# Optimization experiments

Measured on AMD Instinct MI355X. Metric: run time of the kernel, lower is better.

## Reference

```python
import jax, jax.numpy as jnp
import numpy as np

H = 96  # hidden_dim


def _rbf(dist):
    # GaussianSmearing(start=0, stop=10, num_gaussians=16)
    offset = jnp.linspace(0.0, 10.0, 16, dtype=dist.dtype)
    coeff = -0.5 / (10.0 / 15.0) ** 2
    d = dist[:, None] - offset[None, :]
    return jnp.exp(coeff * d * d)


def _gatv2(s, edge, edge_attr, Wl, bl, Wr, br, We, att, bias):
    # PyG GATv2Conv, heads=1: e = leaky_relu(lin_l(x_src)+lin_r(x_tgt)+lin_edge(ea));
    # alpha = segment_softmax(e @ att, tgt); out = scatter_sum(alpha * lin_l(x_src)) + bias
    N = s.shape[0]
    src, tgt = edge[0], edge[1]
    xl = s @ Wl + bl
    xr = s @ Wr + br
    e = jax.nn.leaky_relu(xl[src] + xr[tgt] + edge_attr @ We, 0.2)  # [E,H]
    logits = e @ att  # [E]
    m = jax.ops.segment_max(logits, tgt, num_segments=N)
    a = jnp.exp(logits - m[tgt])
    denom = jax.ops.segment_sum(a, tgt, num_segments=N)
    alpha = a / denom[tgt]
    out = jax.ops.segment_sum(alpha[:, None] * xl[src], tgt, num_segments=N)
    return out + bias


def _encoder(x, edge, pos, Wemb, bemb, gp):
    s0 = x @ Wemb + bemb                      # [N,H]
    s = jax.nn.silu(s0)
    row, col = edge[0], edge[1]
    dist = jnp.linalg.norm(pos[row] - pos[col], axis=-1)
    ea = _rbf(dist)                           # [E,16]
    s = s + jax.nn.silu(_gatv2(s, edge, ea, *gp))
    v = s0.reshape(x.shape[0], -1, 3)[:, :16, :]  # [N,16,3]
    return s, v


def _forward(x_L, pos_L, x_P, pos_P, edge_L, edge_P, cross_src, cross_tgt,
             Wemb_L, bemb_L, Wl_L, bl_L, Wr_L, br_L, We_L, att_L, bias_L,
             Wemb_P, bemb_P, Wl_P, bl_P, Wr_P, br_P, We_P, att_P, bias_P,
             Win, b_in, Wout, bout, Wq, bq, Wk, bk, Wv, bv, W1, b1, W2, b2):
    s_L, v_L = _encoder(x_L, edge_L, pos_L, Wemb_L, bemb_L,
                        (Wl_L, bl_L, Wr_L, br_L, We_L, att_L, bias_L))
    s_P, v_P = _encoder(x_P, edge_P, pos_P, Wemb_P, bemb_P,
                        (Wl_P, bl_P, Wr_P, br_P, We_P, att_P, bias_P))
    # CausalMolSSM: x + out_proj(silu(in_proj(x)).chunk(2)[0])
    h = jax.nn.silu(s_L @ Win + b_in)[:, : 2 * H]
    s_L = s_L + h @ Wout + bout
    # GVPCrossAttention: per-edge gather, global softmax (dim=0 in source), scatter-add
    q = (s_L @ Wq + bq)[cross_tgt]
    k = (s_P @ Wk + bk)[cross_src]
    logits = jnp.sum(q * k, axis=-1) / 8.0     # [E_X]
    attn = jax.nn.softmax(logits, axis=0)      # global softmax over all edges (as in source)
    vmsg = (s_P @ Wv + bv)[cross_src]
    s_L = s_L.at[cross_tgt].add(attn[:, None] * vmsg)
    # head
    return jax.nn.silu(s_L @ W1 + b1) @ W2 + b2  # v_pred [N_L,3]


def setup_inputs() -> dict:
    N_L, N_P = 8192, 32768
    E_L, E_P, E_X = 262144, 524288, 262144
    D_L, D_P = 167, 21
    ks = iter(jax.random.split(jax.random.key(0), 64))

    def w(shape, fan):
        return (jax.random.normal(next(ks), shape, dtype=jnp.float32) / np.sqrt(fan)).astype(jnp.float32)

    inp = {}
    inp['x_L'] = jax.random.normal(next(ks), (N_L, D_L), dtype=jnp.float32)
    inp['pos_L'] = jax.random.normal(next(ks), (N_L, 3), dtype=jnp.float32)
    inp['x_P'] = jax.random.normal(next(ks), (N_P, D_P), dtype=jnp.float32)
    inp['pos_P'] = jax.random.normal(next(ks), (N_P, 3), dtype=jnp.float32)
    inp['edge_L'] = jax.random.randint(next(ks), (2, E_L), 0, N_L)
    inp['edge_P'] = jax.random.randint(next(ks), (2, E_P), 0, N_P)
    inp['cross_src'] = jax.random.randint(next(ks), (E_X,), 0, N_P)
    inp['cross_tgt'] = jax.random.randint(next(ks), (E_X,), 0, N_L)
    for pre, din in (('L', D_L), ('P', D_P)):
        inp[f'Wemb_{pre}'] = w((din, H), din); inp[f'bemb_{pre}'] = w((H,), din)
        inp[f'Wl_{pre}'] = w((H, H), H); inp[f'bl_{pre}'] = w((H,), H)
        inp[f'Wr_{pre}'] = w((H, H), H); inp[f'br_{pre}'] = w((H,), H)
        inp[f'We_{pre}'] = w((16, H), 16)
        inp[f'att_{pre}'] = w((H,), H)
        inp[f'bias_{pre}'] = w((H,), H)
    inp['Win'] = w((H, 4 * H), H); inp['b_in'] = w((4 * H,), H)
    inp['Wout'] = w((2 * H, H), 2 * H); inp['bout'] = w((H,), 2 * H)
    for n in ('q', 'k', 'v'):
        inp[f'W{n}'] = w((H, H), H); inp[f'b{n}'] = w((H,), H)
    inp['W1'] = w((H, H), H); inp['b1'] = w((H,), H)
    inp['W2'] = w((H, 3), H); inp['b2'] = w((3,), H)
    return inp


def reference(x_L, pos_L, x_P, pos_P, edge_L, edge_P, cross_src, cross_tgt,
              Wemb_L, bemb_L, Wl_L, bl_L, Wr_L, br_L, We_L, att_L, bias_L,
              Wemb_P, bemb_P, Wl_P, bl_P, Wr_P, br_P, We_P, att_P, bias_P,
              Win, b_in, Wout, bout, Wq, bq, Wk, bk, Wv, bv, W1, b1, W2, b2):
    return _forward(x_L, pos_L, x_P, pos_P, edge_L, edge_P, cross_src, cross_tgt,
                    Wemb_L, bemb_L, Wl_L, bl_L, Wr_L, br_L, We_L, att_L, bias_L,
                    Wemb_P, bemb_P, Wl_P, bl_P, Wr_P, br_P, We_P, att_P, bias_P,
                    Win, b_in, Wout, bout, Wq, bq, Wk, bk, Wv, bv, W1, b1, W2, b2)
```

## Files before the change

kernel.cpp:

```cpp
#include <hip/hip_runtime.h>

__device__ __forceinline__ float silu_f(float x) { return x / (1.f + __expf(-x)); }

__device__ __forceinline__ void atomicMaxF(float* addr, float val) {
    if (val >= 0.f) atomicMax((int*)addr, __float_as_int(val));
    else            atomicMin((unsigned int*)addr, __float_as_uint(val));
}

__device__ __forceinline__ unsigned short f2bf(float x) {
    unsigned int u = __float_as_uint(x);
    return (unsigned short)((u + 0x7fffu + ((u >> 16) & 1u)) >> 16);
}
__device__ __forceinline__ float bf2f(unsigned short h) {
    return __uint_as_float(((unsigned int)h) << 16);
}
__device__ __forceinline__ float bf_lo(unsigned int u) { return __uint_as_float(u << 16); }
__device__ __forceinline__ float bf_hi(unsigned int u) { return __uint_as_float(u & 0xffff0000u); }
__device__ __forceinline__ float bfdot(unsigned int a, unsigned int b) {
    return bf_lo(a) * bf_lo(b) + bf_hi(a) * bf_hi(b);
}

__global__ void fill_i(int* __restrict__ p, int v, int n) {
    int i = blockIdx.x * blockDim.x + threadIdx.x;
    if (i < n) p[i] = v;
}

__global__ __launch_bounds__(256) void hist_all_kernel(const int* __restrict__ tgtL,
        const int* __restrict__ tgtP, const int* __restrict__ ctgt, int* __restrict__ count,
        int E_L, int E_P, int E_X, int N_L, int N_P) {
    int e = blockIdx.x * blockDim.x + threadIdx.x;
    if (e < E_L) atomicAdd(&count[tgtL[e]], 1);
    else if (e < E_L + E_P) atomicAdd(&count[N_L + tgtP[e - E_L]], 1);
    else if (e < E_L + E_P + E_X) atomicAdd(&count[N_L + N_P + ctgt[e - E_L - E_P]], 1);
}

__global__ __launch_bounds__(256) void scan_blocksum_kernel(const int* __restrict__ count,
                                                            int* __restrict__ bsum, int n) {
    int b = blockIdx.x, t = threadIdx.x;
    int base = b * 4096 + t * 16;
    int s = 0;
#pragma unroll
    for (int k = 0; k < 16; ++k) {
        int idx = base + k;
        s += (idx < n) ? count[idx] : 0;
    }
#pragma unroll
    for (int off = 1; off < 64; off <<= 1) s += __shfl_xor(s, off, 64);
    __shared__ int ws[4];
    int lane = t & 63, wid = t >> 6;
    if (lane == 0) ws[wid] = s;
    __syncthreads();
    if (t == 0) bsum[b] = ws[0] + ws[1] + ws[2] + ws[3];
}

__global__ void scan_top_kernel(int* __restrict__ bsum, int nb, float* __restrict__ csc) {
    if (threadIdx.x == 0) {
        int run = 0;
        for (int i = 0; i < nb; ++i) { int c = bsum[i]; bsum[i] = run; run += c; }
        csc[0] = -3.4e38f; csc[1] = 0.f;
    }
}

__global__ __launch_bounds__(256) void scan_apply_kernel(const int* __restrict__ count,
        const int* __restrict__ bsum, int* __restrict__ rowptr, int* __restrict__ cursor,
        int n, int E) {
    int b = blockIdx.x, t = threadIdx.x;
    int base = b * 4096 + t * 16;
    int v[16];
    int s = 0;
#pragma unroll
    for (int k = 0; k < 16; ++k) {
        int idx = base + k;
        v[k] = (idx < n) ? count[idx] : 0;
        s += v[k];
    }
    int lane = t & 63, wid = t >> 6;
    int inc = s;
#pragma unroll
    for (int off = 1; off < 64; off <<= 1) {
        int o = __shfl_up(inc, off, 64);
        if (lane >= off) inc += o;
    }
    __shared__ int ws[4];
    if (lane == 63) ws[wid] = inc;
    __syncthreads();
    int woff = 0;
    for (int w = 0; w < wid; ++w) woff += ws[w];
    int prefix = bsum[b] + woff + (inc - s);
#pragma unroll
    for (int k = 0; k < 16; ++k) {
        int idx = base + k;
        if (idx < n) { rowptr[idx] = prefix; cursor[idx] = prefix; prefix += v[k]; }
    }
    if (b == 0 && t == 0) rowptr[n] = E;
}

__global__ __launch_bounds__(256) void pre_all_kernel(const int* __restrict__ eL,
        const int* __restrict__ eP, const int* __restrict__ csrc, const int* __restrict__ ctgt,
        const float* __restrict__ posL, const float* __restrict__ posP,
        int* __restrict__ cursor, unsigned int* __restrict__ sdp,
        int E_L, int E_P, int E_X, int N_L, int N_P) {
    int e = blockIdx.x * blockDim.x + threadIdx.x;
    if (e >= E_L + E_P + E_X) return;
    unsigned int pack;
    int node;
    if (e < E_L + E_P) {
        const int* ed; const float* pos; int idx, E, nbase;
        if (e < E_L) { ed = eL; pos = posL; idx = e; E = E_L; nbase = 0; }
        else         { ed = eP; pos = posP; idx = e - E_L; E = E_P; nbase = N_L; }
        int si = ed[idx], ti = ed[E + idx];
        node = nbase + ti;
        float dx = pos[si * 3 + 0] - pos[ti * 3 + 0];
        float dy = pos[si * 3 + 1] - pos[ti * 3 + 1];
        float dz = pos[si * 3 + 2] - pos[ti * 3 + 2];
        float dist = sqrtf(dx * dx + dy * dy + dz * dz);
        int dq = min((int)(dist * 4096.f), 65535);
        pack = (unsigned int)(si + nbase) | ((unsigned int)dq << 16);
    } else {
        int idx = e - E_L - E_P;
        int ti = ctgt[idx];
        pack = (unsigned int)csrc[idx] | ((unsigned int)ti << 16);
        node = N_L + N_P + ti;
    }
    int p = atomicAdd(&cursor[node], 1);
    sdp[p] = pack;
}

__global__ __launch_bounds__(96) void rbf_table_pack_kernel(const float* __restrict__ We_L,
        const float* __restrict__ We_P, unsigned int* __restrict__ T2_L,
        unsigned int* __restrict__ T2_P) {
    int b = blockIdx.x;
    const float* We = (b < 1024) ? We_L : We_P;
    unsigned int* T2 = (b < 1024) ? T2_L : T2_P;
    int i = (b < 1024) ? b : b - 1024;
    int h = threadIdx.x;
    float d0 = (float)i * 0.015625f, d1 = (float)(i + 1) * 0.015625f;
    float a0 = 0.f, a1 = 0.f;
#pragma unroll
    for (int g = 0; g < 16; ++g) {
        float w = We[g * 96 + h];
        float t0 = d0 - 0.66666667f * (float)g;
        float t1 = d1 - 0.66666667f * (float)g;
        a0 += __expf(-1.125f * t0 * t0) * w;
        a1 += __expf(-1.125f * t1 * t1) * w;
    }
    T2[i * 96 + h] = (unsigned int)f2bf(a0) | ((unsigned int)f2bf(a1 - a0) << 16);
}

__global__ __launch_bounds__(256) void gat_all_kernel(const int* __restrict__ rowptr,
        const unsigned int* __restrict__ sdp, const unsigned short* __restrict__ xlb,
        const float* __restrict__ xr,
        const unsigned int* __restrict__ T2_L, const unsigned int* __restrict__ T2_P,
        const float* __restrict__ att_L, const float* __restrict__ att_P,
        const float* __restrict__ bias_L, const float* __restrict__ bias_P,
        float* __restrict__ s_L, float* __restrict__ s_P, int N_L, int Ncomb) {
    int tid = threadIdx.x;
    int l = tid & 31;
    int n = blockIdx.x * 8 + (tid >> 5);
    if (n >= Ncomb) return;
    bool isL = n < N_L;
    const unsigned int* T2 = isL ? T2_L : T2_P;
    const float* att = isL ? att_L : att_P;
    const float* bias = isL ? bias_L : bias_P;
    float* srow = isL ? (s_L + (size_t)n * 96) : (s_P + (size_t)(n - N_L) * 96);
    float att0 = att[l], att1 = att[32 + l], att2 = att[64 + l];
    size_t nb = (size_t)n * 96;
    float xr0 = xr[nb + l], xr1 = xr[nb + 32 + l], xr2 = xr[nb + 64 + l];
    int beg = rowptr[n], end = rowptr[n + 1];
    float m = -3.4e38f, d = 0.f, a0 = 0.f, a1 = 0.f, a2 = 0.f;
    for (int j = beg; j < end; j += 4) {
        unsigned int tp0[4], tp1[4], tp2[4];
        unsigned short xs0[4], xs1[4], xs2[4];
        float ff[4];
#pragma unroll
        for (int k = 0; k < 4; ++k) {
            int jj = min(j + k, end - 1);
            unsigned int u = sdp[jj];
            int src = (int)(u & 0xffffu);
            int dq = (int)(u >> 16);
            int i = dq >> 6;
            ff[k] = (float)(dq & 63) * 0.015625f;
            const unsigned int* tr = T2 + (size_t)i * 96;
            tp0[k] = tr[l]; tp1[k] = tr[32 + l]; tp2[k] = tr[64 + l];
            const unsigned short* xp = xlb + (size_t)src * 96;
            xs0[k] = xp[l]; xs1[k] = xp[32 + l]; xs2[k] = xp[64 + l];
        }
        float y0[4], y1[4], y2[4], lt[4];
#pragma unroll
        for (int k = 0; k < 4; ++k) {
            y0[k] = bf2f(xs0[k]); y1[k] = bf2f(xs1[k]); y2[k] = bf2f(xs2[k]);
            float v0 = y0[k] + xr0 + bf_lo(tp0[k]) + ff[k] * bf_hi(tp0[k]);
            float v1 = y1[k] + xr1 + bf_lo(tp1[k]) + ff[k] * bf_hi(tp1[k]);
            float v2 = y2[k] + xr2 + bf_lo(tp2[k]) + ff[k] * bf_hi(tp2[k]);
            v0 = fmaxf(v0, 0.f) + 0.2f * fminf(v0, 0.f);
            v1 = fmaxf(v1, 0.f) + 0.2f * fminf(v1, 0.f);
            v2 = fmaxf(v2, 0.f) + 0.2f * fminf(v2, 0.f);
            float t = v0 * att0 + v1 * att1 + v2 * att2;
#pragma unroll
            for (int off = 1; off < 32; off <<= 1) t += __shfl_xor(t, off, 64);
            lt[k] = (j + k < end) ? t : -3.4e38f;
        }
        float bm = fmaxf(fmaxf(lt[0], lt[1]), fmaxf(lt[2], lt[3]));
        float nm = fmaxf(m, bm);
        float sc = __expf(m - nm);
        d *= sc; a0 *= sc; a1 *= sc; a2 *= sc;
#pragma unroll
        for (int k = 0; k < 4; ++k) {
            float w = __expf(lt[k] - nm);
            d += w;
            a0 += w * y0[k]; a1 += w * y1[k]; a2 += w * y2[k];
        }
        m = nm;
    }
    float agg0 = (d > 0.f) ? a0 / d : 0.f;
    float agg1 = (d > 0.f) ? a1 / d : 0.f;
    float agg2 = (d > 0.f) ? a2 / d : 0.f;
    srow[l]      += silu_f(agg0 + bias[l]);
    srow[32 + l] += silu_f(agg1 + bias[32 + l]);
    srow[64 + l] += silu_f(agg2 + bias[64 + l]);
}

__global__ __launch_bounds__(256) void cross_logit_e_kernel(const unsigned int* __restrict__ sdX,
        const unsigned short* __restrict__ qnb, const unsigned short* __restrict__ knb,
        float* __restrict__ clog_s, float* __restrict__ csc, int E) {
    int e = blockIdx.x * blockDim.x + threadIdx.x;
    float logit = -3.4e38f;
    if (e < E) {
        unsigned int u = sdX[e];
        int src = (int)(u & 0xffffu);
        int tgt = (int)(u >> 16);
        const uint4* q4 = (const uint4*)(qnb + (size_t)tgt * 96);
        const uint4* k4 = (const uint4*)(knb + (size_t)src * 96);
        float acc = 0.f;
#pragma unroll
        for (int i = 0; i < 12; ++i) {
            uint4 qa = q4[i], ka = k4[i];
            acc += bfdot(qa.x, ka.x) + bfdot(qa.y, ka.y) + bfdot(qa.z, ka.z) + bfdot(qa.w, ka.w);
        }
        logit = acc * 0.125f;
        clog_s[e] = logit;
    }
    __shared__ float red[256];
    red[threadIdx.x] = logit; __syncthreads();
    for (int s = 128; s > 0; s >>= 1) {
        if (threadIdx.x < s) red[threadIdx.x] = fmaxf(red[threadIdx.x], red[threadIdx.x + s]);
        __syncthreads();
    }
    if (threadIdx.x == 0) atomicMaxF(&csc[0], red[0]);
}

__global__ __launch_bounds__(256) void cross_denom_kernel(const float* __restrict__ clog_s,
                                                          float* __restrict__ csc, int E) {
    int e = blockIdx.x * blockDim.x + threadIdx.x;
    float a = 0.f;
    float mg = csc[0];
    if (e < E) a = __expf(clog_s[e] - mg);
    __shared__ float red[256];
    red[threadIdx.x] = a; __syncthreads();
    for (int s = 128; s > 0; s >>= 1) {
        if (threadIdx.x < s) red[threadIdx.x] += red[threadIdx.x + s];
        __syncthreads();
    }
    if (threadIdx.x == 0) atomicAdd(&csc[1], red[0]);
}

__global__ __launch_bounds__(256) void cross_apply_v4_kernel(const int* __restrict__ rowptr,
        const unsigned int* __restrict__ sdp, const float* __restrict__ clog_s,
        const unsigned short* __restrict__ vnb, const float* __restrict__ csc,
        float* __restrict__ sL, int N, int baseX) {
    int tid = threadIdx.x;
    int l = tid & 31;
    int n = blockIdx.x * 8 + (tid >> 5);
    if (n >= N) return;
    int beg = rowptr[n], end = rowptr[n + 1];
    if (beg == end) return;
    float M = csc[0], invD = 1.f / csc[1];
    float a0 = 0.f, a1 = 0.f, a2 = 0.f;
    for (int j = beg; j < end; j += 4) {
        unsigned short v0[4], v1[4], v2[4]; float w[4];
#pragma unroll
        for (int k = 0; k < 4; ++k) {
            int jj = min(j + k, end - 1);
            int src = (int)(sdp[jj] & 0xffffu);
            const unsigned short* vp = vnb + (size_t)src * 96;
            v0[k] = vp[l]; v1[k] = vp[32 + l]; v2[k] = vp[64 + l];
            w[k] = (j + k < end) ? __expf(clog_s[jj - baseX] - M) : 0.f;
        }
#pragma unroll
        for (int k = 0; k < 4; ++k) {
            a0 += w[k] * bf2f(v0[k]); a1 += w[k] * bf2f(v1[k]); a2 += w[k] * bf2f(v2[k]);
        }
    }
    size_t nb = (size_t)n * 96;
    sL[nb + l]      += a0 * invD;
    sL[nb + 32 + l] += a1 * invD;
    sL[nb + 64 + l] += a2 * invD;
}


__global__ __launch_bounds__(192) void enc_all_kernel(
        const float* __restrict__ x_L, const float* __restrict__ x_P,
        const float* __restrict__ WembL, const float* __restrict__ bembL,
        const float* __restrict__ WembP, const float* __restrict__ bembP,
        const float* __restrict__ WlL, const float* __restrict__ blL,
        const float* __restrict__ WrL, const float* __restrict__ brL,
        const float* __restrict__ WlP, const float* __restrict__ blP,
        const float* __restrict__ WrP, const float* __restrict__ brP,
        float* __restrict__ s_L, float* __restrict__ s_P,
        unsigned short* __restrict__ xlb, float* __restrict__ xr,
        int N_L, int N_P, int D_L, int D_P, int BL) {
    __shared__ float xs[16 * 167];
    __shared__ float ss[16 * 96];
    int b = blockIdx.x;
    bool isL = b < BL;
    const float* x    = isL ? x_L : x_P;
    const float* Wemb = isL ? WembL : WembP;
    const float* bemb = isL ? bembL : bembP;
    const float* Wl   = isL ? WlL : WlP;
    const float* bl   = isL ? blL : blP;
    const float* Wr   = isL ? WrL : WrP;
    const float* br   = isL ? brL : brP;
    float* sOut = isL ? s_L : s_P;
    int N = isL ? N_L : N_P;
    int D = isL ? D_L : D_P;
    int n0 = (isL ? b : b - BL) * 16;
    int cbase = isL ? 0 : N_L;
    int t = threadIdx.x, half = t / 96, h = t - half * 96;
    for (int i = t; i < 16 * D; i += 192) {
        int r = i / D, dd = i - r * D, nn = n0 + r;
        xs[i] = (nn < N) ? x[(size_t)nn * D + dd] : 0.f;
    }
    __syncthreads();
    float acc[8]; float bb = bemb[h];
#pragma unroll
    for (int r = 0; r < 8; ++r) acc[r] = bb;
    const float* xp = &xs[half * 8 * D];
    for (int dd = 0; dd < D; ++dd) {
        float w = Wemb[dd * 96 + h];
#pragma unroll
        for (int r = 0; r < 8; ++r) acc[r] += xp[r * D + dd] * w;
    }
#pragma unroll
    for (int r = 0; r < 8; ++r) {
        int nn = n0 + half * 8 + r;
        float v = silu_f(acc[r]);
        if (nn < N) sOut[(size_t)nn * 96 + h] = v;
        ss[(half * 8 + r) * 96 + h] = v;
    }
    __syncthreads();
    const float* sp = &ss[half * 8 * 96];
    float a1[8], a2[8];
    float bb1 = bl[h], bb2 = br[h];
#pragma unroll
    for (int r = 0; r < 8; ++r) { a1[r] = bb1; a2[r] = bb2; }
    for (int k = 0; k < 96; ++k) {
        float w1 = Wl[k * 96 + h], w2 = Wr[k * 96 + h];
#pragma unroll
        for (int r = 0; r < 8; ++r) { float v = sp[r * 96 + k]; a1[r] += v * w1; a2[r] += v * w2; }
    }
#pragma unroll
    for (int r = 0; r < 8; ++r) {
        int nn = n0 + half * 8 + r;
        if (nn < N) {
            xlb[(size_t)(cbase + nn) * 96 + h] = f2bf(a1[r]);
            xr[(size_t)(cbase + nn) * 96 + h] = a2[r];
        }
    }
}

__global__ __launch_bounds__(192) void qkv_all_kernel(
        const float* __restrict__ s_L, const float* __restrict__ s_P,
        const float* __restrict__ Wq, const float* __restrict__ bq,
        const float* __restrict__ Wk, const float* __restrict__ bk,
        const float* __restrict__ Wv, const float* __restrict__ bv,
        unsigned short* __restrict__ qnb, unsigned short* __restrict__ knb,
        unsigned short* __restrict__ vnb, int N_L, int N_P, int BL) {
    __shared__ float xs[16 * 96];
    int b = blockIdx.x;
    bool isL = b < BL;
    const float* s = isL ? s_L : s_P;
    int N = isL ? N_L : N_P;
    int n0 = (isL ? b : b - BL) * 16;
    int t = threadIdx.x, half = t / 96, h = t - half * 96;
    for (int i = t; i < 16 * 96; i += 192) {
        int r = i / 96, c = i - r * 96, nn = n0 + r;
        xs[i] = (nn < N) ? s[(size_t)nn * 96 + c] : 0.f;
    }
    __syncthreads();
    const float* xp = &xs[half * 8 * 96];
    if (isL) {
        float a1[8]; float bb1 = bq[h];
#pragma unroll
        for (int r = 0; r < 8; ++r) a1[r] = bb1;
        for (int k = 0; k < 96; ++k) {
            float w1 = Wq[k * 96 + h];
#pragma unroll
            for (int r = 0; r < 8; ++r) a1[r] += xp[r * 96 + k] * w1;
        }
#pragma unroll
        for (int r = 0; r < 8; ++r) {
            int nn = n0 + half * 8 + r;
            if (nn < N) qnb[(size_t)nn * 96 + h] = f2bf(a1[r]);
        }
    } else {
        float a1[8], a2[8];
        float bb1 = bk[h], bb2 = bv[h];
#pragma unroll
        for (int r = 0; r < 8; ++r) { a1[r] = bb1; a2[r] = bb2; }
        for (int k = 0; k < 96; ++k) {
            float w1 = Wk[k * 96 + h], w2 = Wv[k * 96 + h];
#pragma unroll
            for (int r = 0; r < 8; ++r) { float v = xp[r * 96 + k]; a1[r] += v * w1; a2[r] += v * w2; }
        }
#pragma unroll
        for (int r = 0; r < 8; ++r) {
            int nn = n0 + half * 8 + r;
            if (nn < N) {
                knb[(size_t)nn * 96 + h] = f2bf(a1[r]);
                vnb[(size_t)nn * 96 + h] = f2bf(a2[r]);
            }
        }
    }
}

__global__ __launch_bounds__(192) void ssm2_kernel(float* __restrict__ sL,
        const float* __restrict__ Win, const float* __restrict__ b_in,
        const float* __restrict__ Wout, const float* __restrict__ bout, int N) {
    __shared__ float row[4 * 96];
    __shared__ float u[4 * 192];
    __shared__ float pu[4 * 96];
    int t = threadIdx.x;
    int n0 = blockIdx.x * 4;
    for (int i = t; i < 4 * 96; i += 192) {
        int r = i / 96, c = i - r * 96, nn = n0 + r;
        row[i] = (nn < N) ? sL[(size_t)nn * 96 + c] : 0.f;
    }
    __syncthreads();
    float acc[4]; float bb = b_in[t];
#pragma unroll
    for (int r = 0; r < 4; ++r) acc[r] = bb;
    for (int k = 0; k < 96; ++k) {
        float w = Win[k * 384 + t];
#pragma unroll
        for (int r = 0; r < 4; ++r) acc[r] += row[r * 96 + k] * w;
    }
#pragma unroll
    for (int r = 0; r < 4; ++r) u[r * 192 + t] = silu_f(acc[r]);
    __syncthreads();
    int half = t / 96, h = t - half * 96;
    float d[4] = {0.f, 0.f, 0.f, 0.f};
    int j0 = half * 96;
    for (int j = j0; j < j0 + 96; ++j) {
        float w = Wout[j * 96 + h];
#pragma unroll
        for (int r = 0; r < 4; ++r) d[r] += u[r * 192 + j] * w;
    }
    if (half == 1) {
#pragma unroll
        for (int r = 0; r < 4; ++r) pu[r * 96 + h] = d[r];
    }
    __syncthreads();
    if (half == 0) {
        float bo = bout[h];
#pragma unroll
        for (int r = 0; r < 4; ++r) {
            int nn = n0 + r;
            if (nn < N) sL[(size_t)nn * 96 + h] = row[r * 96 + h] + bo + d[r] + pu[r * 96 + h];
        }
    }
}

__global__ __launch_bounds__(192) void head2_kernel(const float* __restrict__ sL,
        const float* __restrict__ W1, const float* __restrict__ b1,
        const float* __restrict__ W2, const float* __restrict__ b2,
        float* __restrict__ out, int N) {
    __shared__ float buf[16 * 96];
    int t = threadIdx.x, half = t / 96, h = t - half * 96;
    int n0 = blockIdx.x * 16;
    for (int i = t; i < 16 * 96; i += 192) {
        int r = i / 96, c = i - r * 96, nn = n0 + r;
        buf[i] = (nn < N) ? sL[(size_t)nn * 96 + c] : 0.f;
    }
    __syncthreads();
    int rbase = half * 8;
    float a[8]; float bb = b1[h];
#pragma unroll
    for (int r = 0; r < 8; ++r) a[r] = bb;
    for (int k = 0; k < 96; ++k) {
        float w = W1[k * 96 + h];
#pragma unroll
        for (int r = 0; r < 8; ++r) a[r] += buf[(rbase + r) * 96 + k] * w;
    }
    __syncthreads();
#pragma unroll
    for (int r = 0; r < 8; ++r) buf[(rbase + r) * 96 + h] = silu_f(a[r]);
    __syncthreads();
    if (t < 48) {
        int r = t / 3, c = t - r * 3;
        float o = b2[c];
        for (int j = 0; j < 96; ++j) o += buf[r * 96 + j] * W2[j * 3 + c];
        int nn = n0 + r;
        if (nn < N) out[nn * 3 + c] = o;
    }
}

static inline int cdiv(int a, int b) { return (a + b - 1) / b; }

extern "C" void kernel_launch(void* const* d_in, const int* in_sizes, int n_in,
                              void* d_out, int out_size, void* d_ws, size_t ws_size,
                              hipStream_t stream) {
    const float* x_L   = (const float*)d_in[0];
    const float* pos_L = (const float*)d_in[1];
    const float* x_P   = (const float*)d_in[2];
    const float* pos_P = (const float*)d_in[3];
    const int* edge_L = (const int*)d_in[4];
    const int* edge_P = (const int*)d_in[5];
    const int* csrc   = (const int*)d_in[6];
    const int* ctgt   = (const int*)d_in[7];
    const float *Wemb_L = (const float*)d_in[8],  *bemb_L = (const float*)d_in[9];
    const float *Wl_L = (const float*)d_in[10], *bl_L = (const float*)d_in[11];
    const float *Wr_L = (const float*)d_in[12], *br_L = (const float*)d_in[13];
    const float *We_L = (const float*)d_in[14], *att_L = (const float*)d_in[15], *bias_L = (const float*)d_in[16];
    const float *Wemb_P = (const float*)d_in[17], *bemb_P = (const float*)d_in[18];
    const float *Wl_P = (const float*)d_in[19], *bl_P = (const float*)d_in[20];
    const float *Wr_P = (const float*)d_in[21], *br_P = (const float*)d_in[22];
    const float *We_P = (const float*)d_in[23], *att_P = (const float*)d_in[24], *bias_P = (const float*)d_in[25];
    const float *Win = (const float*)d_in[26], *b_in = (const float*)d_in[27];
    const float *Wout = (const float*)d_in[28], *bout = (const float*)d_in[29];
    const float *Wq = (const float*)d_in[30], *bq = (const float*)d_in[31];
    const float *Wk = (const float*)d_in[32], *bk = (const float*)d_in[33];
    const float *Wv = (const float*)d_in[34], *bv = (const float*)d_in[35];
    const float *W1 = (const float*)d_in[36], *b1 = (const float*)d_in[37];
    const float *W2 = (const float*)d_in[38], *b2 = (const float*)d_in[39];

    const int N_L = in_sizes[1] / 3;
    const int N_P = in_sizes[3] / 3;
    const int E_L = in_sizes[4] / 2;
    const int E_P = in_sizes[5] / 2;
    const int E_X = in_sizes[6];
    const int D_L = in_sizes[0] / N_L;
    const int D_P = in_sizes[2] / N_P;
    const int Ncomb = N_L + N_P;
    const int Ntot = N_L + N_P + N_L;
    const int Etot = E_L + E_P + E_X;
    const int baseX = E_L + E_P;

    float* ws = (float*)d_ws;
    float*          s_L    = ws;
    float*          s_P    = s_L + (size_t)N_L * 96;
    float*          xr     = s_P + (size_t)N_P * 96;
    unsigned short* xlb    = (unsigned short*)(xr + (size_t)Ncomb * 96);
    unsigned short* knb    = xlb + (size_t)Ncomb * 96;
    unsigned short* vnb    = knb + (size_t)N_P * 96;
    unsigned short* qnb    = vnb + (size_t)N_P * 96;
    unsigned int*   sdp    = (unsigned int*)(qnb + (size_t)N_L * 96);
    float*          clog_s = (float*)(sdp + (size_t)Etot);
    unsigned int*   T2_L   = (unsigned int*)(clog_s + (size_t)E_X);
    unsigned int*   T2_P   = T2_L + 1024 * 96;
    int*            rowptr = (int*)(T2_P + 1024 * 96);
    int*            count  = rowptr + (size_t)Ntot + 1;
    int*            cursor = count + (size_t)Ntot;
    float*          csc    = (float*)(cursor + (size_t)Ntot);
    int*            bsum   = (int*)(csc + 2);

    const int BL = cdiv(N_L, 16), BP = cdiv(N_P, 16);

    rbf_table_pack_kernel<<<2048, 96, 0, stream>>>(We_L, We_P, T2_L, T2_P);
    fill_i<<<cdiv(Ntot, 256), 256, 0, stream>>>(count, 0, Ntot);
    hist_all_kernel<<<cdiv(Etot, 256), 256, 0, stream>>>(edge_L + E_L, edge_P + E_P, ctgt,
        count, E_L, E_P, E_X, N_L, N_P);
    scan_blocksum_kernel<<<cdiv(Ntot, 4096), 256, 0, stream>>>(count, bsum, Ntot);
    scan_top_kernel<<<1, 64, 0, stream>>>(bsum, cdiv(Ntot, 4096), csc);
    scan_apply_kernel<<<cdiv(Ntot, 4096), 256, 0, stream>>>(count, bsum, rowptr, cursor, Ntot, Etot);
    pre_all_kernel<<<cdiv(Etot, 256), 256, 0, stream>>>(edge_L, edge_P, csrc, ctgt,
        pos_L, pos_P, cursor, sdp, E_L, E_P, E_X, N_L, N_P);

    enc_all_kernel<<<BL + BP, 192, 0, stream>>>(x_L, x_P, Wemb_L, bemb_L, Wemb_P, bemb_P,
        Wl_L, bl_L, Wr_L, br_L, Wl_P, bl_P, Wr_P, br_P,
        s_L, s_P, xlb, xr, N_L, N_P, D_L, D_P, BL);

    gat_all_kernel<<<cdiv(Ncomb, 8), 256, 0, stream>>>(rowptr, sdp, xlb, xr, T2_L, T2_P,
        att_L, att_P, bias_L, bias_P, s_L, s_P, N_L, Ncomb);

    ssm2_kernel<<<cdiv(N_L, 4), 192, 0, stream>>>(s_L, Win, b_in, Wout, bout, N_L);

    qkv_all_kernel<<<BL + BP, 192, 0, stream>>>(s_L, s_P, Wq, bq, Wk, bk, Wv, bv,
        qnb, knb, vnb, N_L, N_P, BL);
    cross_logit_e_kernel<<<cdiv(E_X, 256), 256, 0, stream>>>(sdp + (size_t)baseX, qnb, knb,
        clog_s, csc, E_X);
    cross_denom_kernel<<<cdiv(E_X, 256), 256, 0, stream>>>(clog_s, csc, E_X);
    cross_apply_v4_kernel<<<cdiv(N_L, 8), 256, 0, stream>>>(rowptr + N_L + N_P, sdp,
        clog_s, vnb, csc, s_L, N_L, baseX);

    head2_kernel<<<cdiv(N_L, 16), 192, 0, stream>>>(s_L, W1, b1, W2, b2, (float*)d_out, N_L);
}
```

Baseline: 505.4 us.

## Register-tile dense node GEMMs 4x4 with float4 weights; store xr as bf16

Rewrites the per-node dense matmul kernels (encoder, qkv, SSM, head) so each thread computes a 4-row by 4-column register tile using float4 weight loads, with 32 nodes per block instead of 16. The SSM kernel now handles 8 rows per block and no longer splits the output projection across two halves with a shared-memory reduction. The xr projection is stored as bf16 instead of fp32, which halves its memory traffic in the GAT kernel at some cost in precision. Larger tiles cut redundant weight loads but leave fewer blocks, which may reduce occupancy at small node counts.

Measured after the change: 466.5 us. -7.7%, faster.

```diff
diff --git a/kernel.cpp b/kernel.cpp
--- a/kernel.cpp
+++ b/kernel.cpp
@@ -149,7 +149,7 @@
 
 __global__ __launch_bounds__(256) void gat_all_kernel(const int* __restrict__ rowptr,
         const unsigned int* __restrict__ sdp, const unsigned short* __restrict__ xlb,
-        const float* __restrict__ xr,
+        const unsigned short* __restrict__ xrb,
         const unsigned int* __restrict__ T2_L, const unsigned int* __restrict__ T2_P,
         const float* __restrict__ att_L, const float* __restrict__ att_P,
         const float* __restrict__ bias_L, const float* __restrict__ bias_P,
@@ -165,7 +165,7 @@
     float* srow = isL ? (s_L + (size_t)n * 96) : (s_P + (size_t)(n - N_L) * 96);
     float att0 = att[l], att1 = att[32 + l], att2 = att[64 + l];
     size_t nb = (size_t)n * 96;
-    float xr0 = xr[nb + l], xr1 = xr[nb + 32 + l], xr2 = xr[nb + 64 + l];
+    float xr0 = bf2f(xrb[nb + l]), xr1 = bf2f(xrb[nb + 32 + l]), xr2 = bf2f(xrb[nb + 64 + l]);
     int beg = rowptr[n], end = rowptr[n + 1];
     float m = -3.4e38f, d = 0.f, a0 = 0.f, a1 = 0.f, a2 = 0.f;
     for (int j = beg; j < end; j += 4) {
@@ -307,10 +307,10 @@
         const float* __restrict__ WlP, const float* __restrict__ blP,
         const float* __restrict__ WrP, const float* __restrict__ brP,
         float* __restrict__ s_L, float* __restrict__ s_P,
-        unsigned short* __restrict__ xlb, float* __restrict__ xr,
+        unsigned short* __restrict__ xlb, unsigned short* __restrict__ xrb,
         int N_L, int N_P, int D_L, int D_P, int BL) {
-    __shared__ float xs[16 * 167];
-    __shared__ float ss[16 * 96];
+    __shared__ float xs[32 * 167];
+    __shared__ float ss[32 * 96];
     int b = blockIdx.x;
     bool isL = b < BL;
     const float* x    = isL ? x_L : x_P;
@@ -323,47 +323,65 @@
     float* sOut = isL ? s_L : s_P;
     int N = isL ? N_L : N_P;
     int D = isL ? D_L : D_P;
-    int n0 = (isL ? b : b - BL) * 16;
+    int n0 = (isL ? b : b - BL) * 32;
     int cbase = isL ? 0 : N_L;
-    int t = threadIdx.x, half = t / 96, h = t - half * 96;
-    for (int i = t; i < 16 * D; i += 192) {
+    int t = threadIdx.x;
+    int hg = t % 24, h4 = hg * 4;
+    int rg = t / 24;
+    for (int i = t; i < 32 * D; i += 192) {
         int r = i / D, dd = i - r * D, nn = n0 + r;
         xs[i] = (nn < N) ? x[(size_t)nn * D + dd] : 0.f;
     }
     __syncthreads();
-    float acc[8]; float bb = bemb[h];
-#pragma unroll
-    for (int r = 0; r < 8; ++r) acc[r] = bb;
-    const float* xp = &xs[half * 8 * D];
+    float4 be = *(const float4*)&bemb[h4];
+    float acc[4][4];
+#pragma unroll
+    for (int r = 0; r < 4; ++r) { acc[r][0] = be.x; acc[r][1] = be.y; acc[r][2] = be.z; acc[r][3] = be.w; }
+    const float* xrow = &xs[rg * 4 * D];
     for (int dd = 0; dd < D; ++dd) {
-        float w = Wemb[dd * 96 + h];
-#pragma unroll
-        for (int r = 0; r < 8; ++r) acc[r] += xp[r * D + dd] * w;
-    }
-#pragma unroll
-    for (int r = 0; r < 8; ++r) {
-        int nn = n0 + half * 8 + r;
-        float v = silu_f(acc[r]);
-        if (nn < N) sOut[(size_t)nn * 96 + h] = v;
-        ss[(half * 8 + r) * 96 + h] = v;
-    }
-    __syncthreads();
-    const float* sp = &ss[half * 8 * 96];
-    float a1[8], a2[8];
-    float bb1 = bl[h], bb2 = br[h];
-#pragma unroll
-    for (int r = 0; r < 8; ++r) { a1[r] = bb1; a2[r] = bb2; }
+        float4 w = *(const float4*)&Wemb[dd * 96 + h4];
+#pragma unroll
+        for (int r = 0; r < 4; ++r) {
+            float xv = xrow[r * D + dd];
+            acc[r][0] += xv * w.x; acc[r][1] += xv * w.y;
+            acc[r][2] += xv * w.z; acc[r][3] += xv * w.w;
+        }
+    }
+#pragma unroll
+    for (int r = 0; r < 4; ++r) {
+        int row = rg * 4 + r, nn = n0 + row;
+        float4 v = make_float4(silu_f(acc[r][0]), silu_f(acc[r][1]),
+                               silu_f(acc[r][2]), silu_f(acc[r][3]));
+        *(float4*)&ss[row * 96 + h4] = v;
+        if (nn < N) *(float4*)&sOut[(size_t)nn * 96 + h4] = v;
+    }
+    __syncthreads();
+    float4 b1v = *(const float4*)&bl[h4];
+    float4 b2v = *(const float4*)&br[h4];
+    float a1[4][4], a2[4][4];
+#pragma unroll
+    for (int r = 0; r < 4; ++r) {
+        a1[r][0] = b1v.x; a1[r][1] = b1v.y; a1[r][2] = b1v.z; a1[r][3] = b1v.w;
+        a2[r][0] = b2v.x; a2[r][1] = b2v.y; a2[r][2] = b2v.z; a2[r][3] = b2v.w;
+    }
+    const float* srow = &ss[rg * 4 * 96];
     for (int k = 0; k < 96; ++k) {
-        float w1 = Wl[k * 96 + h], w2 = Wr[k * 96 + h];
-#pragma unroll
-        for (int r = 0; r < 8; ++r) { float v = sp[r * 96 + k]; a1[r] += v * w1; a2[r] += v * w2; }
-    }
-#pragma unroll
-    for (int r = 0; r < 8; ++r) {
-        int nn = n0 + half * 8 + r;
+        float4 w1 = *(const float4*)&Wl[k * 96 + h4];
+        float4 w2 = *(const float4*)&Wr[k * 96 + h4];
+#pragma unroll
+        for (int r = 0; r < 4; ++r) {
+            float xv = srow[r * 96 + k];
+            a1[r][0] += xv * w1.x; a1[r][1] += xv * w1.y; a1[r][2] += xv * w1.z; a1[r][3] += xv * w1.w;
+            a2[r][0] += xv * w2.x; a2[r][1] += xv * w2.y; a2[r][2] += xv * w2.z; a2[r][3] += xv * w2.w;
+        }
+    }
+#pragma unroll
+    for (int r = 0; r < 4; ++r) {
+        int nn = n0 + rg * 4 + r;
         if (nn < N) {
-            xlb[(size_t)(cbase + nn) * 96 + h] = f2bf(a1[r]);
-            xr[(size_t)(cbase + nn) * 96 + h] = a2[r];
+            size_t o = (size_t)(cbase + nn) * 96 + h4;
+            *(ushort4*)&xlb[o] = make_ushort4(f2bf(a1[r][0]), f2bf(a1[r][1]), f2bf(a1[r][2]), f2bf(a1[r][3]));
+            *(ushort4*)&xrb[o] = make_ushort4(f2bf(a2[r][0]), f2bf(a2[r][1]), f2bf(a2[r][2]), f2bf(a2[r][3]));
         }
     }
 }
@@ -375,130 +393,171 @@
         const float* __restrict__ Wv, const float* __restrict__ bv,
         unsigned short* __restrict__ qnb, unsigned short* __restrict__ knb,
         unsigned short* __restrict__ vnb, int N_L, int N_P, int BL) {
-    __shared__ float xs[16 * 96];
+    __shared__ float xs[32 * 96];
     int b = blockIdx.x;
     bool isL = b < BL;
     const float* s = isL ? s_L : s_P;
     int N = isL ? N_L : N_P;
-    int n0 = (isL ? b : b - BL) * 16;
-    int t = threadIdx.x, half = t / 96, h = t - half * 96;
-    for (int i = t; i < 16 * 96; i += 192) {
+    int n0 = (isL ? b : b - BL) * 32;
+    int t = threadIdx.x;
+    int hg = t % 24, h4 = hg * 4;
+    int rg = t / 24;
+    for (int i = t; i < 32 * 96; i += 192) {
         int r = i / 96, c = i - r * 96, nn = n0 + r;
         xs[i] = (nn < N) ? s[(size_t)nn * 96 + c] : 0.f;
     }
     __syncthreads();
-    const float* xp = &xs[half * 8 * 96];
+    const float* srow = &xs[rg * 4 * 96];
     if (isL) {
-        float a1[8]; float bb1 = bq[h];
-#pragma unroll
-        for (int r = 0; r < 8; ++r) a1[r] = bb1;
+        float4 bb = *(const float4*)&bq[h4];
+        float a1[4][4];
+#pragma unroll
+        for (int r = 0; r < 4; ++r) { a1[r][0] = bb.x; a1[r][1] = bb.y; a1[r][2] = bb.z; a1[r][3] = bb.w; }
         for (int k = 0; k < 96; ++k) {
-            float w1 = Wq[k * 96 + h];
-#pragma unroll
-            for (int r = 0; r < 8; ++r) a1[r] += xp[r * 96 + k] * w1;
-        }
-#pragma unroll
-        for (int r = 0; r < 8; ++r) {
-            int nn = n0 + half * 8 + r;
-            if (nn < N) qnb[(size_t)nn * 96 + h] = f2bf(a1[r]);
+            float4 w = *(const float4*)&Wq[k * 96 + h4];
+#pragma unroll
+            for (int r = 0; r < 4; ++r) {
+                float xv = srow[r * 96 + k];
+                a1[r][0] += xv * w.x; a1[r][1] += xv * w.y; a1[r][2] += xv * w.z; a1[r][3] += xv * w.w;
+            }
+        }
+#pragma unroll
+        for (int r = 0; r < 4; ++r) {
+            int nn = n0 + rg * 4 + r;
+            if (nn < N)
+                *(ushort4*)&qnb[(size_t)nn * 96 + h4] =
+                    make_ushort4(f2bf(a1[r][0]), f2bf(a1[r][1]), f2bf(a1[r][2]), f2bf(a1[r][3]));
         }
     } else {
-        float a1[8], a2[8];
-        float bb1 = bk[h], bb2 = bv[h];
-#pragma unroll
-        for (int r = 0; r < 8; ++r) { a1[r] = bb1; a2[r] = bb2; }
+        float4 bb1 = *(const float4*)&bk[h4];
+        float4 bb2 = *(const float4*)&bv[h4];
+        float a1[4][4], a2[4][4];
+#pragma unroll
+        for (int r = 0; r < 4; ++r) {
+            a1[r][0] = bb1.x; a1[r][1] = bb1.y; a1[r][2] = bb1.z; a1[r][3] = bb1.w;
+            a2[r][0] = bb2.x; a2[r][1] = bb2.y; a2[r][2] = bb2.z; a2[r][3] = bb2.w;
+        }
         for (int k = 0; k < 96; ++k) {
-            float w1 = Wk[k * 96 + h], w2 = Wv[k * 96 + h];
-#pragma unroll
-            for (int r = 0; r < 8; ++r) { float v = xp[r * 96 + k]; a1[r] += v * w1; a2[r] += v * w2; }
-        }
-#pragma unroll
-        for (int r = 0; r < 8; ++r) {
-            int nn = n0 + half * 8 + r;
+            float4 w1 = *(const float4*)&Wk[k * 96 + h4];
+            float4 w2 = *(const float4*)&Wv[k * 96 + h4];
+#pragma unroll
+            for (int r = 0; r < 4; ++r) {
+                float xv = srow[r * 96 + k];
+                a1[r][0] += xv * w1.x; a1[r][1] += xv * w1.y; a1[r][2] += xv * w1.z; a1[r][3] += xv * w1.w;
+                a2[r][0] += xv * w2.x; a2[r][1] += xv * w2.y; a2[r][2] += xv * w2.z; a2[r][3] += xv * w2.w;
+            }
+        }
+#pragma unroll
+        for (int r = 0; r < 4; ++r) {
+            int nn = n0 + rg * 4 + r;
             if (nn < N) {
-                knb[(size_t)nn * 96 + h] = f2bf(a1[r]);
-                vnb[(size_t)nn * 96 + h] = f2bf(a2[r]);
+                *(ushort4*)&knb[(size_t)nn * 96 + h4] =
+                    make_ushort4(f2bf(a1[r][0]), f2bf(a1[r][1]), f2bf(a1[r][2]), f2bf(a1[r][3]));
+                *(ushort4*)&vnb[(size_t)nn * 96 + h4] =
+                    make_ushort4(f2bf(a2[r][0]), f2bf(a2[r][1]), f2bf(a2[r][2]), f2bf(a2[r][3]));
             }
         }
     }
 }
 
-__global__ __launch_bounds__(192) void ssm2_kernel(float* __restrict__ sL,
+__global__ __launch_bounds__(192) void ssm3_kernel(float* __restrict__ sL,
         const float* __restrict__ Win, const float* __restrict__ b_in,
         const float* __restrict__ Wout, const float* __restrict__ bout, int N) {
-    __shared__ float row[4 * 96];
-    __shared__ float u[4 * 192];
-    __shared__ float pu[4 * 96];
+    __shared__ float row[8 * 96];
+    __shared__ float u[8 * 192];
     int t = threadIdx.x;
-    int n0 = blockIdx.x * 4;
-    for (int i = t; i < 4 * 96; i += 192) {
+    int n0 = blockIdx.x * 8;
+    for (int i = t; i < 8 * 96; i += 192) {
         int r = i / 96, c = i - r * 96, nn = n0 + r;
         row[i] = (nn < N) ? sL[(size_t)nn * 96 + c] : 0.f;
     }
     __syncthreads();
-    float acc[4]; float bb = b_in[t];
-#pragma unroll
-    for (int r = 0; r < 4; ++r) acc[r] = bb;
-    for (int k = 0; k < 96; ++k) {
-        float w = Win[k * 384 + t];
-#pragma unroll
-        for (int r = 0; r < 4; ++r) acc[r] += row[r * 96 + k] * w;
-    }
-#pragma unroll
-    for (int r = 0; r < 4; ++r) u[r * 192 + t] = silu_f(acc[r]);
-    __syncthreads();
-    int half = t / 96, h = t - half * 96;
-    float d[4] = {0.f, 0.f, 0.f, 0.f};
-    int j0 = half * 96;
-    for (int j = j0; j < j0 + 96; ++j) {
-        float w = Wout[j * 96 + h];
-#pragma unroll
-        for (int r = 0; r < 4; ++r) d[r] += u[r * 192 + j] * w;
-    }
-    if (half == 1) {
-#pragma unroll
-        for (int r = 0; r < 4; ++r) pu[r * 96 + h] = d[r];
-    }
-    __syncthreads();
-    if (half == 0) {
-        float bo = bout[h];
-#pragma unroll
-        for (int r = 0; r < 4; ++r) {
-            int nn = n0 + r;
-            if (nn < N) sL[(size_t)nn * 96 + h] = row[r * 96 + h] + bo + d[r] + pu[r * 96 + h];
-        }
-    }
-}
-
-__global__ __launch_bounds__(192) void head2_kernel(const float* __restrict__ sL,
+    {
+        int cg = t % 48, c4 = cg * 4;
+        int rg = t / 48;
+        float4 bb = *(const float4*)&b_in[c4];
+        float a[2][4];
+#pragma unroll
+        for (int r = 0; r < 2; ++r) { a[r][0] = bb.x; a[r][1] = bb.y; a[r][2] = bb.z; a[r][3] = bb.w; }
+        const float* rr = &row[rg * 2 * 96];
+        for (int k = 0; k < 96; ++k) {
+            float4 w = *(const float4*)&Win[k * 384 + c4];
+#pragma unroll
+            for (int r = 0; r < 2; ++r) {
+                float xv = rr[r * 96 + k];
+                a[r][0] += xv * w.x; a[r][1] += xv * w.y; a[r][2] += xv * w.z; a[r][3] += xv * w.w;
+            }
+        }
+#pragma unroll
+        for (int r = 0; r < 2; ++r) {
+            int ro = rg * 2 + r;
+            u[ro * 192 + c4 + 0] = silu_f(a[r][0]);
+            u[ro * 192 + c4 + 1] = silu_f(a[r][1]);
+            u[ro * 192 + c4 + 2] = silu_f(a[r][2]);
+            u[ro * 192 + c4 + 3] = silu_f(a[r][3]);
+        }
+    }
+    __syncthreads();
+    {
+        int hg = t % 24, h4 = hg * 4;
+        int rg2 = t / 24;
+        float4 bb = *(const float4*)&bout[h4];
+        float a[4] = {bb.x, bb.y, bb.z, bb.w};
+        const float* ur = &u[rg2 * 192];
+        for (int j = 0; j < 192; ++j) {
+            float4 w = *(const float4*)&Wout[j * 96 + h4];
+            float uv = ur[j];
+            a[0] += uv * w.x; a[1] += uv * w.y; a[2] += uv * w.z; a[3] += uv * w.w;
+        }
+        int nn = n0 + rg2;
+        if (nn < N) {
+            float4 rv = *(const float4*)&row[rg2 * 96 + h4];
+            *(float4*)&sL[(size_t)nn * 96 + h4] =
+                make_float4(rv.x + a[0], rv.y + a[1], rv.z + a[2], rv.w + a[3]);
+        }
+    }
+}
+
+__global__ __launch_bounds__(192) void head3_kernel(const float* __restrict__ sL,
         const float* __restrict__ W1, const float* __restrict__ b1,
         const float* __restrict__ W2, const float* __restrict__ b2,
         float* __restrict__ out, int N) {
-    __shared__ float buf[16 * 96];
-    int t = threadIdx.x, half = t / 96, h = t - half * 96;
-    int n0 = blockIdx.x * 16;
-    for (int i = t; i < 16 * 96; i += 192) {
+    __shared__ float buf[32 * 96];
+    __shared__ float tt[32 * 96];
+    int t = threadIdx.x;
+    int n0 = blockIdx.x * 32;
+    for (int i = t; i < 32 * 96; i += 192) {
         int r = i / 96, c = i - r * 96, nn = n0 + r;
         buf[i] = (nn < N) ? sL[(size_t)nn * 96 + c] : 0.f;
     }
     __syncthreads();
-    int rbase = half * 8;
-    float a[8]; float bb = b1[h];
-#pragma unroll
-    for (int r = 0; r < 8; ++r) a[r] = bb;
+    int hg = t % 24, h4 = hg * 4;
+    int rg = t / 24;
+    float4 bb = *(const float4*)&b1[h4];
+    float a[4][4];
+#pragma unroll
+    for (int r = 0; r < 4; ++r) { a[r][0] = bb.x; a[r][1] = bb.y; a[r][2] = bb.z; a[r][3] = bb.w; }
+    const float* srow = &buf[rg * 4 * 96];
     for (int k = 0; k < 96; ++k) {
-        float w = W1[k * 96 + h];
-#pragma unroll
-        for (int r = 0; r < 8; ++r) a[r] += buf[(rbase + r) * 96 + k] * w;
-    }
-    __syncthreads();
-#pragma unroll
-    for (int r = 0; r < 8; ++r) buf[(rbase + r) * 96 + h] = silu_f(a[r]);
-    __syncthreads();
-    if (t < 48) {
+        float4 w = *(const float4*)&W1[k * 96 + h4];
+#pragma unroll
+        for (int r = 0; r < 4; ++r) {
+            float xv = srow[r * 96 + k];
+            a[r][0] += xv * w.x; a[r][1] += xv * w.y; a[r][2] += xv * w.z; a[r][3] += xv * w.w;
+        }
+    }
+#pragma unroll
+    for (int r = 0; r < 4; ++r) {
+        int row = rg * 4 + r;
+        *(float4*)&tt[row * 96 + h4] = make_float4(silu_f(a[r][0]), silu_f(a[r][1]),
+                                                   silu_f(a[r][2]), silu_f(a[r][3]));
+    }
+    __syncthreads();
+    if (t < 96) {
         int r = t / 3, c = t - r * 3;
         float o = b2[c];
-        for (int j = 0; j < 96; ++j) o += buf[r * 96 + j] * W2[j * 3 + c];
+        const float* tr = &tt[r * 96];
+        for (int j = 0; j < 96; ++j) o += tr[j] * W2[j * 3 + c];
         int nn = n0 + r;
         if (nn < N) out[nn * 3 + c] = o;
     }
@@ -548,8 +607,8 @@
     float* ws = (float*)d_ws;
     float*          s_L    = ws;
     float*          s_P    = s_L + (size_t)N_L * 96;
-    float*          xr     = s_P + (size_t)N_P * 96;
-    unsigned short* xlb    = (unsigned short*)(xr + (size_t)Ncomb * 96);
+    unsigned short* xrb    = (unsigned short*)(s_P + (size_t)N_P * 96);
+    unsigned short* xlb    = xrb + (size_t)Ncomb * 96;
     unsigned short* knb    = xlb + (size_t)Ncomb * 96;
     unsigned short* vnb    = knb + (size_t)N_P * 96;
     unsigned short* qnb    = vnb + (size_t)N_P * 96;
@@ -563,7 +622,7 @@
     float*          csc    = (float*)(cursor + (size_t)Ntot);
     int*            bsum   = (int*)(csc + 2);
 
-    const int BL = cdiv(N_L, 16), BP = cdiv(N_P, 16);
+    const int BL = cdiv(N_L, 32), BP = cdiv(N_P, 32);
 
     rbf_table_pack_kernel<<<2048, 96, 0, stream>>>(We_L, We_P, T2_L, T2_P);
     fill_i<<<cdiv(Ntot, 256), 256, 0, stream>>>(count, 0, Ntot);
@@ -577,12 +636,12 @@
 
     enc_all_kernel<<<BL + BP, 192, 0, stream>>>(x_L, x_P, Wemb_L, bemb_L, Wemb_P, bemb_P,
         Wl_L, bl_L, Wr_L, br_L, Wl_P, bl_P, Wr_P, br_P,
-        s_L, s_P, xlb, xr, N_L, N_P, D_L, D_P, BL);
-
-    gat_all_kernel<<<cdiv(Ncomb, 8), 256, 0, stream>>>(rowptr, sdp, xlb, xr, T2_L, T2_P,
+        s_L, s_P, xlb, xrb, N_L, N_P, D_L, D_P, BL);
+
+    gat_all_kernel<<<cdiv(Ncomb, 8), 256, 0, stream>>>(rowptr, sdp, xlb, xrb, T2_L, T2_P,
         att_L, att_P, bias_L, bias_P, s_L, s_P, N_L, Ncomb);
 
-    ssm2_kernel<<<cdiv(N_L, 4), 192, 0, stream>>>(s_L, Win, b_in, Wout, bout, N_L);
+    ssm3_kernel<<<cdiv(N_L, 8), 192, 0, stream>>>(s_L, Win, b_in, Wout, bout, N_L);
 
     qkv_all_kernel<<<BL + BP, 192, 0, stream>>>(s_L, s_P, Wq, bq, Wk, bk, Wv, bv,
         qnb, knb, vnb, N_L, N_P, BL);
@@ -592,5 +651,5 @@
     cross_apply_v4_kernel<<<cdiv(N_L, 8), 256, 0, stream>>>(rowptr + N_L + N_P, sdp,
         clog_s, vnb, csc, s_L, N_L, baseX);
 
-    head2_kernel<<<cdiv(N_L, 16), 192, 0, stream>>>(s_L, W1, b1, W2, b2, (float*)d_out, N_L);
-}
+    head3_kernel<<<cdiv(N_L, 32), 192, 0, stream>>>(s_L, W1, b1, W2, b2, (float*)d_out, N_L);
+}
```
